# Performance work log

Hardware: AMD Instinct MI355X
Metric: run time of the kernel (lower is better)

## Reference

```python
import jax, jax.numpy as jnp
import numpy as np

B, NP, NT = 16, 4096, 77
QD, CD, H, DH = 512, 768, 8, 64
INNER = H * DH


def setup_inputs() -> dict:
    key = jax.random.key(0)
    ks = jax.random.split(key, 8)
    s = 0.02
    return {
        "x": jax.random.normal(ks[0], (B, NP, QD), jnp.float32),
        "context": jax.random.normal(ks[1], (B, NT, CD), jnp.float32),
        "mask": jnp.ones((B, NP, NT), jnp.int32),
        "Wq": jax.random.normal(ks[2], (QD, INNER), jnp.float32) * s,
        "Wk": jax.random.normal(ks[3], (CD, INNER), jnp.float32) * s,
        "Wv": jax.random.normal(ks[4], (CD, INNER), jnp.float32) * s,
        "Wo": jax.random.normal(ks[5], (INNER, QD), jnp.float32) * s,
        "bo": jnp.zeros((QD,), jnp.float32),
    }


def reference(x, context, mask, Wq, Wk, Wv, Wo, bo):
    scale = 1.0 / jnp.sqrt(jnp.asarray(DH, x.dtype))
    # projections -> (B, H, N, DH)
    q = (x @ Wq).reshape(B, NP, H, DH).transpose(0, 2, 1, 3)
    k = (context @ Wk).reshape(B, NT, H, DH).transpose(0, 2, 1, 3)
    v = (context @ Wv).reshape(B, NT, H, DH).transpose(0, 2, 1, 3)
    # scores (B, H, NP, NT)
    attn = jnp.einsum("bhqd,bhkd->bhqk", q, k) * scale
    attn = jnp.where(mask[:, None, :, :] == 0, -jnp.inf, attn)
    attn = jax.nn.softmax(attn, axis=-1)
    out = jnp.einsum("bhqk,bhkd->bhqd", attn, v)
    out = out.transpose(0, 2, 1, 3).reshape(B, NP, INNER)
    return out @ Wo + bo
```

## Files before the change

kernel.cpp:

```cpp
#include <hip/hip_runtime.h>


typedef _Float16 half_t;
typedef _Float16 half8 __attribute__((ext_vector_type(8)));
typedef float f32x4 __attribute__((ext_vector_type(4)));
typedef unsigned int u32;

#define NB 16
#define NP 4096
#define NT 77
#define NTP 96
#define QD 512
#define CD 768
#define NH 8
#define DH 64
#define INNER 512
#define MKV (NB * NT)

__device__ __forceinline__ void stage16(const void* g, void* l) {
    __builtin_amdgcn_global_load_lds((const __attribute__((address_space(1))) u32*)g,
                                     (__attribute__((address_space(3))) u32*)l, 16, 0, 0);
}

__device__ __forceinline__ f32x4 mfma16(half8 a, half8 b, f32x4 c) {
    return __builtin_amdgcn_mfma_f32_16x16x32_f16(a, b, c, 0, 0, 0);
}

__global__ __launch_bounds__(256) void kTrans2(const float* __restrict__ in0,
                                               const float* __restrict__ in1,
                                               half_t* __restrict__ out0,
                                               half_t* __restrict__ out1,
                                               int K, int N) {
    const float* in = blockIdx.z ? in1 : in0;
    half_t* out = blockIdx.z ? out1 : out0;
    __shared__ float tile[32][33];
    int tx = threadIdx.x & 31, ty = threadIdx.x >> 5;
    int kb = blockIdx.y * 32, nb = blockIdx.x * 32;
    for (int r = ty; r < 32; r += 8)
        tile[r][tx] = in[(size_t)(kb + r) * N + nb + tx];
    __syncthreads();
    for (int r = ty; r < 32; r += 8)
        out[(size_t)(nb + r) * K + kb + tx] = (half_t)tile[tx][r];
}

__global__ __launch_bounds__(256) void kKVproj(const float* __restrict__ Ctx,
                                               const half_t* __restrict__ WkT,
                                               const half_t* __restrict__ WvT,
                                               half_t* __restrict__ Kp,
                                               half_t* __restrict__ VTp) {
    __shared__ alignas(16) half_t As[64 * 96];
    __shared__ alignas(16) half_t Bs[128 * 96];
    const int t = threadIdx.x, w = t >> 6, lane = t & 63;
    const int c0 = lane & 15, q4 = lane >> 4;
    const int m0 = blockIdx.y * 64;
    const int n0g = blockIdx.x * 128;
    const int z = n0g >= 512;
    const int n0 = n0g - z * 512;
    const half_t* WT = z ? WvT : WkT;

    f32x4 acc[4][2] = {};
    for (int k0 = 0; k0 < CD; k0 += 96) {
        for (int q = 0; q < 3; ++q) {
            int u = q * 256 + t;
            int row = u / 12, h8 = (u % 12) * 8;
            int gr = m0 + row; if (gr > MKV - 1) gr = MKV - 1;
            const float* src = Ctx + (size_t)gr * CD + k0 + h8;
            f32x4 f0 = *(const f32x4*)src;
            f32x4 f1 = *(const f32x4*)(src + 4);
            half8 hv;
            for (int e = 0; e < 4; ++e) { hv[e] = (half_t)f0[e]; hv[4 + e] = (half_t)f1[e]; }
            *(half8*)&As[row * 96 + h8] = hv;
        }
        for (int q = 0; q < 6; ++q) {
            int c = q * 256 + t;
            stage16(WT + (size_t)(n0 + c / 12) * CD + k0 + (c % 12) * 8, &Bs[c * 8]);
        }
        __syncthreads();
        for (int ks = 0; ks < 3; ++ks) {
            half8 a[4], b[2];
            for (int i = 0; i < 4; ++i)
                a[i] = *(const half8*)&As[(16 * i + c0) * 96 + ks * 32 + q4 * 8];
            for (int j = 0; j < 2; ++j)
                b[j] = *(const half8*)&Bs[(w * 32 + 16 * j + c0) * 96 + ks * 32 + q4 * 8];
            for (int i = 0; i < 4; ++i)
                for (int j = 0; j < 2; ++j)
                    acc[i][j] = mfma16(a[i], b[j], acc[i][j]);
        }
        __syncthreads();
    }
    for (int i = 0; i < 4; ++i)
        for (int j = 0; j < 2; ++j)
            for (int r = 0; r < 4; ++r) {
                int row = m0 + 16 * i + q4 * 4 + r;
                if (row >= MKV) continue;
                int col = n0 + w * 32 + 16 * j + c0;
                int b = row / NT, tt = row - b * NT;
                int h = col >> 6, d = col & 63;
                half_t v = (half_t)acc[i][j][r];
                if (!z) Kp[(((size_t)b * NH + h) * NTP + tt) * DH + d] = v;
                else    VTp[(((size_t)b * NH + h) * DH + d) * NTP + tt] = v;
            }
}

__global__ __launch_bounds__(256) void kQproj(const float* __restrict__ X,
                                              const half_t* __restrict__ WqT,
                                              half_t* __restrict__ Q) {
    __shared__ alignas(16) half_t As[128 * 32];
    __shared__ alignas(16) half_t Bs[128 * 32];
    const int t = threadIdx.x, w = t >> 6, lane = t & 63;
    const int c0 = lane & 15, q4 = lane >> 4;
    const int wm = w & 1, wn = w >> 1;
    const int m0 = blockIdx.y * 128, n0 = blockIdx.x * 128;

    f32x4 acc[4][4] = {};
    for (int k0 = 0; k0 < QD; k0 += 32) {
        for (int q = 0; q < 2; ++q) {
            int u = q * 256 + t;
            int row = u >> 2, h8 = (u & 3) * 8;
            const float* src = X + (size_t)(m0 + row) * QD + k0 + h8;
            f32x4 f0 = *(const f32x4*)src;
            f32x4 f1 = *(const f32x4*)(src + 4);
            half8 hv;
            for (int e = 0; e < 4; ++e) { hv[e] = (half_t)f0[e]; hv[4 + e] = (half_t)f1[e]; }
            *(half8*)&As[row * 32 + h8] = hv;
        }
        for (int q = 0; q < 2; ++q) {
            int c = q * 256 + t;
            stage16(WqT + (size_t)(n0 + (c >> 2)) * QD + k0 + (c & 3) * 8, &Bs[c * 8]);
        }
        __syncthreads();
        half8 a[4];
        for (int i = 0; i < 4; ++i)
            a[i] = *(const half8*)&As[(wm * 64 + 16 * i + c0) * 32 + q4 * 8];
        for (int j = 0; j < 4; ++j) {
            half8 bv = *(const half8*)&Bs[(wn * 64 + 16 * j + c0) * 32 + q4 * 8];
            for (int i = 0; i < 4; ++i)
                acc[i][j] = mfma16(a[i], bv, acc[i][j]);
        }
        __syncthreads();
    }
    for (int i = 0; i < 4; ++i)
        for (int j = 0; j < 4; ++j)
            for (int r = 0; r < 4; ++r) {
                int row = m0 + wm * 64 + 16 * i + q4 * 4 + r;
                int col = n0 + wn * 64 + 16 * j + c0;
                Q[(size_t)row * INNER + col] = (half_t)acc[i][j][r];
            }
}

__global__ __launch_bounds__(256) void kAttn(half_t* __restrict__ Q,
                                             const half_t* __restrict__ Kp,
                                             const half_t* __restrict__ VTp,
                                             const int* __restrict__ mask) {
    __shared__ alignas(16) half_t Qs[128 * 104];
    __shared__ alignas(16) half_t Ks[NTP * 72];
    __shared__ alignas(16) half_t VTs[DH * 104];
    const int t = threadIdx.x, w = t >> 6, lane = t & 63;
    const int c0 = lane & 15, q4 = lane >> 4;
    const int qt = blockIdx.x, h = blockIdx.y, b = blockIdx.z;
    const int q0 = qt * 128;
    const size_t qbase = ((size_t)b * NP + q0) * INNER + h * DH;

    for (int q = 0; q < 4; ++q) {
        int c = q * 256 + t, m = c >> 3, k8 = (c & 7) * 8;
        *(uint4*)&Qs[m * 104 + k8] = *(const uint4*)(Q + qbase + (size_t)m * INNER + k8);
    }
    const half_t* Kh = Kp + ((size_t)b * NH + h) * NTP * DH;
    for (int q = 0; q < 3; ++q) {
        int c = q * 256 + t, r = c >> 3, k8 = (c & 7) * 8;
        *(uint4*)&Ks[r * 72 + k8] = *(const uint4*)(Kh + r * DH + k8);
    }
    const half_t* Vh = VTp + ((size_t)b * NH + h) * DH * NTP;
    for (int q = 0; q < 3; ++q) {
        int c = q * 256 + t, r = c / 12, t8 = (c % 12) * 8;
        *(uint4*)&VTs[r * 104 + t8] = *(const uint4*)(Vh + r * NTP + t8);
    }
    __syncthreads();

    const int r0 = w * 32;
    f32x4 sacc[2][6] = {};
    for (int ks = 0; ks < 2; ++ks) {
        half8 a0 = *(const half8*)&Qs[(r0 + c0) * 104 + ks * 32 + q4 * 8];
        half8 a1 = *(const half8*)&Qs[(r0 + 16 + c0) * 104 + ks * 32 + q4 * 8];
        for (int j = 0; j < 6; ++j) {
            half8 bv = *(const half8*)&Ks[(16 * j + c0) * 72 + ks * 32 + q4 * 8];
            sacc[0][j] = mfma16(a0, bv, sacc[0][j]);
            sacc[1][j] = mfma16(a1, bv, sacc[1][j]);
        }
    }

    for (int i = 0; i < 2; ++i)
        for (int r = 0; r < 4; ++r) {
            int qrow = r0 + 16 * i + q4 * 4 + r;
            const int* mrow = mask + ((size_t)b * NP + q0 + qrow) * NT;
            float sv[6];
            for (int j = 0; j < 6; ++j) {
                int tt = 16 * j + c0;
                float s = sacc[i][j][r] * 0.125f;
                bool valid = (tt < NT) && (mrow[tt < NT ? tt : NT - 1] != 0);
                sv[j] = valid ? s : -1e30f;
            }
            float mx = sv[0];
            for (int j = 1; j < 6; ++j) mx = fmaxf(mx, sv[j]);
            for (int d = 1; d < 16; d <<= 1) mx = fmaxf(mx, __shfl_xor(mx, d));
            float pv[6], sum = 0.f;
            for (int j = 0; j < 6; ++j) { pv[j] = __expf(sv[j] - mx); sum += pv[j]; }
            for (int d = 1; d < 16; d <<= 1) sum += __shfl_xor(sum, d);
            float inv = 1.0f / sum;
            for (int j = 0; j < 6; ++j)
                Qs[qrow * 104 + 16 * j + c0] = (half_t)(pv[j] * inv);
        }
    __syncthreads();

    f32x4 oacc[2][4] = {};
    for (int ks = 0; ks < 3; ++ks) {
        half8 a0 = *(const half8*)&Qs[(r0 + c0) * 104 + ks * 32 + q4 * 8];
        half8 a1 = *(const half8*)&Qs[(r0 + 16 + c0) * 104 + ks * 32 + q4 * 8];
        for (int j = 0; j < 4; ++j) {
            half8 bv = *(const half8*)&VTs[(16 * j + c0) * 104 + ks * 32 + q4 * 8];
            oacc[0][j] = mfma16(a0, bv, oacc[0][j]);
            oacc[1][j] = mfma16(a1, bv, oacc[1][j]);
        }
    }
    for (int i = 0; i < 2; ++i)
        for (int j = 0; j < 4; ++j)
            for (int r = 0; r < 4; ++r) {
                int qrow = r0 + 16 * i + q4 * 4 + r;
                int d = 16 * j + c0;
                Q[qbase + (size_t)qrow * INNER + d] = (half_t)oacc[i][j][r];
            }
}

__global__ __launch_bounds__(256) void kOproj(const half_t* __restrict__ AO,
                                              const half_t* __restrict__ WoT,
                                              const float* __restrict__ bo,
                                              float* __restrict__ out) {
    __shared__ alignas(16) half_t As[128 * 32];
    __shared__ alignas(16) half_t Bs[128 * 32];
    const int t = threadIdx.x, w = t >> 6, lane = t & 63;
    const int c0 = lane & 15, q4 = lane >> 4;
    const int wm = w & 1, wn = w >> 1;
    const int m0 = blockIdx.y * 128, n0 = blockIdx.x * 128;

    float bj[4];
    for (int j = 0; j < 4; ++j) bj[j] = bo[n0 + wn * 64 + 16 * j + c0];

    f32x4 acc[4][4] = {};
    for (int k0 = 0; k0 < INNER; k0 += 32) {
        for (int q = 0; q < 2; ++q) {
            int c = q * 256 + t;
            stage16(AO + (size_t)(m0 + (c >> 2)) * INNER + k0 + (c & 3) * 8, &As[c * 8]);
        }
        for (int q = 0; q < 2; ++q) {
            int c = q * 256 + t;
            stage16(WoT + (size_t)(n0 + (c >> 2)) * INNER + k0 + (c & 3) * 8, &Bs[c * 8]);
        }
        __syncthreads();
        half8 a[4];
        for (int i = 0; i < 4; ++i)
            a[i] = *(const half8*)&As[(wm * 64 + 16 * i + c0) * 32 + q4 * 8];
        for (int j = 0; j < 4; ++j) {
            half8 bv = *(const half8*)&Bs[(wn * 64 + 16 * j + c0) * 32 + q4 * 8];
            for (int i = 0; i < 4; ++i)
                acc[i][j] = mfma16(a[i], bv, acc[i][j]);
        }
        __syncthreads();
    }
    for (int i = 0; i < 4; ++i)
        for (int j = 0; j < 4; ++j)
            for (int r = 0; r < 4; ++r) {
                int row = m0 + wm * 64 + 16 * i + q4 * 4 + r;
                int col = n0 + wn * 64 + 16 * j + c0;
                out[(size_t)row * QD + col] = acc[i][j][r] + bj[j];
            }
}

extern "C" void kernel_launch(void* const* d_in, const int* in_sizes, int n_in,
                              void* d_out, int out_size, void* d_ws, size_t ws_size,
                              hipStream_t stream) {
    const float* x   = (const float*)d_in[0];
    const float* ctx = (const float*)d_in[1];
    const int*   msk = (const int*)d_in[2];
    const float* Wq  = (const float*)d_in[3];
    const float* Wk  = (const float*)d_in[4];
    const float* Wv  = (const float*)d_in[5];
    const float* Wo  = (const float*)d_in[6];
    const float* bo  = (const float*)d_in[7];
    float* out = (float*)d_out;

    half_t* Qws = (half_t*)d_ws;
    half_t* WqT = Qws + (size_t)NB * NP * INNER;
    half_t* WoT = WqT + (size_t)QD * INNER;
    half_t* WkT = WoT + (size_t)INNER * QD;
    half_t* WvT = WkT + (size_t)INNER * CD;
    half_t* Kp  = WvT + (size_t)INNER * CD;
    half_t* VTp = Kp + (size_t)NB * NH * NTP * DH;

    kTrans2<<<dim3(INNER / 32, QD / 32, 2), 256, 0, stream>>>(Wq, Wo, WqT, WoT, QD, INNER);
    kTrans2<<<dim3(INNER / 32, CD / 32, 2), 256, 0, stream>>>(Wk, Wv, WkT, WvT, CD, INNER);
    hipMemsetAsync(Kp, 0, (size_t)NB * NH * (NTP * DH + DH * NTP) * sizeof(half_t), stream);
    kKVproj<<<dim3(8, 20), 256, 0, stream>>>(ctx, WkT, WvT, Kp, VTp);
    kQproj<<<dim3(INNER / 128, NB * NP / 128), 256, 0, stream>>>(x, WqT, Qws);
    kAttn<<<dim3(NP / 128, NH, NB), 256, 0, stream>>>(Qws, Kp, VTp, msk);
    kOproj<<<dim3(QD / 128, NB * NP / 128), 256, 0, stream>>>(Qws, WoT, bo, out);
}
```

Baseline: 443.4 us.

## Swizzle LDS tiles, widen GEMM K-tiles, remap blocks across XCDs, drop attention barrier

The projection GEMMs now stage 64-wide K tiles into LDS with an XOR row swizzle on the 16-byte chunks. This is meant to remove bank conflicts on the MFMA operand reads and halve the number of barrier-separated K iterations. The Q and O projections switch to a 1-D grid with a block-id remap, so that consecutive blocks on the same XCD work on neighbouring M tiles for better L2 reuse. The attention kernel drops the barrier between writing softmax probabilities to LDS and reading them back. That is only safe if each wave reads exclusively the rows it wrote itself, so it risks a race.

Result: faster. 407.4 us (-8.1%).

```diff
diff --git a/kernel.cpp b/kernel.cpp
--- a/kernel.cpp
+++ b/kernel.cpp
@@ -48,10 +48,11 @@
                                                const half_t* __restrict__ WvT,
                                                half_t* __restrict__ Kp,
                                                half_t* __restrict__ VTp) {
-    __shared__ alignas(16) half_t As[64 * 96];
-    __shared__ alignas(16) half_t Bs[128 * 96];
+    __shared__ alignas(16) half_t As[64 * 64];
+    __shared__ alignas(16) half_t Bs[128 * 64];
     const int t = threadIdx.x, w = t >> 6, lane = t & 63;
     const int c0 = lane & 15, q4 = lane >> 4;
+    const int rx = c0 & 7;
     const int m0 = blockIdx.y * 64;
     const int n0g = blockIdx.x * 128;
     const int z = n0g >= 512;
@@ -59,29 +60,32 @@
     const half_t* WT = z ? WvT : WkT;
 
     f32x4 acc[4][2] = {};
-    for (int k0 = 0; k0 < CD; k0 += 96) {
-        for (int q = 0; q < 3; ++q) {
-            int u = q * 256 + t;
-            int row = u / 12, h8 = (u % 12) * 8;
+    for (int k0 = 0; k0 < CD; k0 += 64) {
+        for (int q = 0; q < 2; ++q) {
+            int c = q * 256 + t;
+            int row = c >> 3, ch = c & 7;
             int gr = m0 + row; if (gr > MKV - 1) gr = MKV - 1;
-            const float* src = Ctx + (size_t)gr * CD + k0 + h8;
+            const float* src = Ctx + (size_t)gr * CD + k0 + ch * 8;
             f32x4 f0 = *(const f32x4*)src;
             f32x4 f1 = *(const f32x4*)(src + 4);
             half8 hv;
             for (int e = 0; e < 4; ++e) { hv[e] = (half_t)f0[e]; hv[4 + e] = (half_t)f1[e]; }
-            *(half8*)&As[row * 96 + h8] = hv;
-        }
-        for (int q = 0; q < 6; ++q) {
-            int c = q * 256 + t;
-            stage16(WT + (size_t)(n0 + c / 12) * CD + k0 + (c % 12) * 8, &Bs[c * 8]);
-        }
-        __syncthreads();
-        for (int ks = 0; ks < 3; ++ks) {
+            *(half8*)&As[row * 64 + ((ch ^ (row & 7)) * 8)] = hv;
+        }
+        for (int q = 0; q < 4; ++q) {
+            int c = q * 256 + t;
+            int row = c >> 3, k8 = c & 7;
+            stage16(WT + (size_t)(n0 + row) * CD + k0 + (k8 ^ (row & 7)) * 8, &Bs[c * 8]);
+        }
+        __syncthreads();
+        for (int ks = 0; ks < 2; ++ks) {
+            int ch = ks * 4 + q4;
+            int cx = (ch ^ rx) * 8;
             half8 a[4], b[2];
             for (int i = 0; i < 4; ++i)
-                a[i] = *(const half8*)&As[(16 * i + c0) * 96 + ks * 32 + q4 * 8];
+                a[i] = *(const half8*)&As[(16 * i + c0) * 64 + cx];
             for (int j = 0; j < 2; ++j)
-                b[j] = *(const half8*)&Bs[(w * 32 + 16 * j + c0) * 96 + ks * 32 + q4 * 8];
+                b[j] = *(const half8*)&Bs[(w * 32 + 16 * j + c0) * 64 + cx];
             for (int i = 0; i < 4; ++i)
                 for (int j = 0; j < 2; ++j)
                     acc[i][j] = mfma16(a[i], b[j], acc[i][j]);
@@ -105,37 +109,44 @@
 __global__ __launch_bounds__(256) void kQproj(const float* __restrict__ X,
                                               const half_t* __restrict__ WqT,
                                               half_t* __restrict__ Q) {
-    __shared__ alignas(16) half_t As[128 * 32];
-    __shared__ alignas(16) half_t Bs[128 * 32];
+    __shared__ alignas(16) half_t As[128 * 64];
+    __shared__ alignas(16) half_t Bs[128 * 64];
     const int t = threadIdx.x, w = t >> 6, lane = t & 63;
     const int c0 = lane & 15, q4 = lane >> 4;
+    const int rx = c0 & 7;
     const int wm = w & 1, wn = w >> 1;
-    const int m0 = blockIdx.y * 128, n0 = blockIdx.x * 128;
+    const int bid = blockIdx.x;
+    const int wid = (bid & 7) * 256 + (bid >> 3);
+    const int m0 = (wid >> 2) * 128, n0 = (wid & 3) * 128;
 
     f32x4 acc[4][4] = {};
-    for (int k0 = 0; k0 < QD; k0 += 32) {
-        for (int q = 0; q < 2; ++q) {
-            int u = q * 256 + t;
-            int row = u >> 2, h8 = (u & 3) * 8;
-            const float* src = X + (size_t)(m0 + row) * QD + k0 + h8;
+    for (int k0 = 0; k0 < QD; k0 += 64) {
+        for (int q = 0; q < 4; ++q) {
+            int c = q * 256 + t;
+            int row = c >> 3, ch = c & 7;
+            const float* src = X + (size_t)(m0 + row) * QD + k0 + ch * 8;
             f32x4 f0 = *(const f32x4*)src;
             f32x4 f1 = *(const f32x4*)(src + 4);
             half8 hv;
             for (int e = 0; e < 4; ++e) { hv[e] = (half_t)f0[e]; hv[4 + e] = (half_t)f1[e]; }
-            *(half8*)&As[row * 32 + h8] = hv;
-        }
-        for (int q = 0; q < 2; ++q) {
-            int c = q * 256 + t;
-            stage16(WqT + (size_t)(n0 + (c >> 2)) * QD + k0 + (c & 3) * 8, &Bs[c * 8]);
-        }
-        __syncthreads();
-        half8 a[4];
-        for (int i = 0; i < 4; ++i)
-            a[i] = *(const half8*)&As[(wm * 64 + 16 * i + c0) * 32 + q4 * 8];
-        for (int j = 0; j < 4; ++j) {
-            half8 bv = *(const half8*)&Bs[(wn * 64 + 16 * j + c0) * 32 + q4 * 8];
+            *(half8*)&As[row * 64 + ((ch ^ (row & 7)) * 8)] = hv;
+        }
+        for (int q = 0; q < 4; ++q) {
+            int c = q * 256 + t;
+            int row = c >> 3, k8 = c & 7;
+            stage16(WqT + (size_t)(n0 + row) * QD + k0 + (k8 ^ (row & 7)) * 8, &Bs[c * 8]);
+        }
+        __syncthreads();
+        for (int ks = 0; ks < 2; ++ks) {
+            int cx = ((ks * 4 + q4) ^ rx) * 8;
+            half8 a[4];
             for (int i = 0; i < 4; ++i)
-                acc[i][j] = mfma16(a[i], bv, acc[i][j]);
+                a[i] = *(const half8*)&As[(wm * 64 + 16 * i + c0) * 64 + cx];
+            for (int j = 0; j < 4; ++j) {
+                half8 bv = *(const half8*)&Bs[(wn * 64 + 16 * j + c0) * 64 + cx];
+                for (int i = 0; i < 4; ++i)
+                    acc[i][j] = mfma16(a[i], bv, acc[i][j]);
+            }
         }
         __syncthreads();
     }
@@ -210,7 +221,6 @@
             for (int j = 0; j < 6; ++j)
                 Qs[qrow * 104 + 16 * j + c0] = (half_t)(pv[j] * inv);
         }
-    __syncthreads();
 
     f32x4 oacc[2][4] = {};
     for (int ks = 0; ks < 3; ++ks) {
@@ -227,7 +237,7 @@
             for (int r = 0; r < 4; ++r) {
                 int qrow = r0 + 16 * i + q4 * 4 + r;
                 int d = 16 * j + c0;
-                Q[qbase + (size_t)qrow * INNER + d] = (half_t)oacc[i][j][r];
+                Q[qbase + (size_t)qrow * INNER + d] = (half_t)oacc[2 > 1 ? i : i][j][r];
             }
 }
 
@@ -235,34 +245,42 @@
                                               const half_t* __restrict__ WoT,
                                               const float* __restrict__ bo,
                                               float* __restrict__ out) {
-    __shared__ alignas(16) half_t As[128 * 32];
-    __shared__ alignas(16) half_t Bs[128 * 32];
+    __shared__ alignas(16) half_t As[128 * 64];
+    __shared__ alignas(16) half_t Bs[128 * 64];
     const int t = threadIdx.x, w = t >> 6, lane = t & 63;
     const int c0 = lane & 15, q4 = lane >> 4;
+    const int rx = c0 & 7;
     const int wm = w & 1, wn = w >> 1;
-    const int m0 = blockIdx.y * 128, n0 = blockIdx.x * 128;
+    const int bid = blockIdx.x;
+    const int wid = (bid & 7) * 256 + (bid >> 3);
+    const int m0 = (wid >> 2) * 128, n0 = (wid & 3) * 128;
 
     float bj[4];
     for (int j = 0; j < 4; ++j) bj[j] = bo[n0 + wn * 64 + 16 * j + c0];
 
     f32x4 acc[4][4] = {};
-    for (int k0 = 0; k0 < INNER; k0 += 32) {
-        for (int q = 0; q < 2; ++q) {
-            int c = q * 256 + t;
-            stage16(AO + (size_t)(m0 + (c >> 2)) * INNER + k0 + (c & 3) * 8, &As[c * 8]);
-        }
-        for (int q = 0; q < 2; ++q) {
-            int c = q * 256 + t;
-            stage16(WoT + (size_t)(n0 + (c >> 2)) * INNER + k0 + (c & 3) * 8, &Bs[c * 8]);
-        }
-        __syncthreads();
-        half8 a[4];
-        for (int i = 0; i < 4; ++i)
-            a[i] = *(const half8*)&As[(wm * 64 + 16 * i + c0) * 32 + q4 * 8];
-        for (int j = 0; j < 4; ++j) {
-            half8 bv = *(const half8*)&Bs[(wn * 64 + 16 * j + c0) * 32 + q4 * 8];
+    for (int k0 = 0; k0 < INNER; k0 += 64) {
+        for (int q = 0; q < 4; ++q) {
+            int c = q * 256 + t;
+            int row = c >> 3, k8 = c & 7;
+            stage16(AO + (size_t)(m0 + row) * INNER + k0 + (k8 ^ (row & 7)) * 8, &As[c * 8]);
+        }
+        for (int q = 0; q < 4; ++q) {
+            int c = q * 256 + t;
+            int row = c >> 3, k8 = c & 7;
+            stage16(WoT + (size_t)(n0 + row) * INNER + k0 + (k8 ^ (row & 7)) * 8, &Bs[c * 8]);
+        }
+        __syncthreads();
+        for (int ks = 0; ks < 2; ++ks) {
+            int cx = ((ks * 4 + q4) ^ rx) * 8;
+            half8 a[4];
             for (int i = 0; i < 4; ++i)
-                acc[i][j] = mfma16(a[i], bv, acc[i][j]);
+                a[i] = *(const half8*)&As[(wm * 64 + 16 * i + c0) * 64 + cx];
+            for (int j = 0; j < 4; ++j) {
+                half8 bv = *(const half8*)&Bs[(wn * 64 + 16 * j + c0) * 64 + cx];
+                for (int i = 0; i < 4; ++i)
+                    acc[i][j] = mfma16(a[i], bv, acc[i][j]);
+            }
         }
         __syncthreads();
     }
@@ -300,7 +318,7 @@
     kTrans2<<<dim3(INNER / 32, CD / 32, 2), 256, 0, stream>>>(Wk, Wv, WkT, WvT, CD, INNER);
     hipMemsetAsync(Kp, 0, (size_t)NB * NH * (NTP * DH + DH * NTP) * sizeof(half_t), stream);
     kKVproj<<<dim3(8, 20), 256, 0, stream>>>(ctx, WkT, WvT, Kp, VTp);
-    kQproj<<<dim3(INNER / 128, NB * NP / 128), 256, 0, stream>>>(x, WqT, Qws);
+    kQproj<<<dim3(2048), 256, 0, stream>>>(x, WqT, Qws);
     kAttn<<<dim3(NP / 128, NH, NB), 256, 0, stream>>>(Qws, Kp, VTp, msk);
-    kOproj<<<dim3(QD / 128, NB * NP / 128), 256, 0, stream>>>(Qws, WoT, bo, out);
-}
+    kOproj<<<dim3(2048), 256, 0, stream>>>(Qws, WoT, bo, out);
+}
```
